# Kernel optimization log

Measured on AMD Instinct MI355X. Metric: run time of the kernel, lower is better.

## Reference

```python
import jax, jax.numpy as jnp
import numpy as np

D_MODEL = 512
N_HEADS = 8
NUM_NODES = 20
EPS = 1e-5

def _layer_norm(x, g, b):
    mu = jnp.mean(x, axis=-1, keepdims=True)
    var = jnp.var(x, axis=-1, keepdims=True)
    return (x - mu) * jax.lax.rsqrt(var + EPS) * g + b

def _conv1d(x_bcn, w_oik):
    # x: [B, C, N], w: [O, I, K], padding = K//2 (same)
    k = w_oik.shape[-1]
    p = k // 2
    return jax.lax.conv_general_dilated(
        x_bcn, w_oik, window_strides=(1,), padding=[(p, p)],
        dimension_numbers=('NCH', 'OIH', 'NCH'))

def setup_inputs() -> dict:
    key = jax.random.key(0)
    ks = jax.random.split(key, 6)
    B, N, D, H = 4096, NUM_NODES, D_MODEL, N_HEADS
    x = jax.random.normal(ks[0], (B, N, D), dtype=jnp.float32)
    s = 1.0 / np.sqrt(D * 3)
    Wq = jax.random.normal(ks[1], (D, D, 3), dtype=jnp.float32) * s
    Wk = jax.random.normal(ks[2], (D, D, 3), dtype=jnp.float32) * s
    Wv = jax.random.normal(ks[3], (D, D, 3), dtype=jnp.float32) * s
    rel_table = jax.random.normal(ks[4], (2 * N - 1, H), dtype=jnp.float32) * 0.02
    Wo = jax.random.normal(ks[5], (D, D), dtype=jnp.float32) * (1.0 / np.sqrt(D))
    bo = jnp.zeros((D,), dtype=jnp.float32)
    ones = jnp.ones((D,), dtype=jnp.float32)
    zeros = jnp.zeros((D,), dtype=jnp.float32)
    return {"x": x, "Wq": Wq, "Wk": Wk, "Wv": Wv,
            "lnq_g": ones, "lnq_b": zeros, "lnk_g": ones, "lnk_b": zeros,
            "lnv_g": ones, "lnv_b": zeros,
            "rel_table": rel_table, "Wo": Wo, "bo": bo}

def reference(x, Wq, Wk, Wv, lnq_g, lnq_b, lnk_g, lnk_b, lnv_g, lnv_b, rel_table, Wo, bo):
    B, N, D = x.shape
    H = N_HEADS
    dk = D // H
    x_p = jnp.transpose(x, (0, 2, 1))  # [B, D, N]

    def proj(W, g, b):
        c = _conv1d(x_p, W)                      # [B, D, N]
        c = _layer_norm(jnp.transpose(c, (0, 2, 1)), g, b)  # [B, N, D]
        return x + c                              # residual

    q = proj(Wq, lnq_g, lnq_b)
    k = proj(Wk, lnk_g, lnk_b)
    v = proj(Wv, lnv_g, lnv_b)

    q = q.reshape(B, N, H, dk).transpose(0, 2, 1, 3)  # [B,H,N,dk]
    k = k.reshape(B, N, H, dk).transpose(0, 2, 1, 3)
    v = v.reshape(B, N, H, dk).transpose(0, 2, 1, 3)

    scale = 1.0 / np.sqrt(dk)
    scores = jnp.einsum('bhnd,bhmd->bhnm', q, k) * scale  # [B,H,N,N]

    # relative position bias: index[i,j] = i - j + N - 1
    coords = jnp.arange(N)
    rel_idx = coords[:, None] - coords[None, :] + (N - 1)   # [N,N]
    rel_bias = rel_table[rel_idx]                            # [N,N,H]
    rel_bias = jnp.transpose(rel_bias, (2, 0, 1))[None]      # [1,H,N,N]
    scores = scores + rel_bias

    attn = jax.nn.softmax(scores, axis=-1)
    out = jnp.einsum('bhnm,bhmd->bhnd', attn, v)             # [B,H,N,dk]
    out = out.transpose(0, 2, 1, 3).reshape(B, N, D)
    return out @ Wo.T + bo
```

## Files before the change

kernel.cpp:

```cpp
#include <hip/hip_runtime.h>
#include <hip/hip_bf16.h>
#include <stdint.h>
#include <string.h>

typedef __attribute__((ext_vector_type(8))) __bf16 bf16x8;
typedef __attribute__((ext_vector_type(2))) __bf16 bf16x2;
typedef __attribute__((ext_vector_type(4))) float f32x4;
typedef __attribute__((ext_vector_type(16))) float f32x16;

#define B_TOT   4096
#define NN      20
#define DM      512
#define NC1     1536
#define M_TOT   (B_TOT*NN)
#define NPAD    22

__device__ __forceinline__ void async_copy16(const __bf16* g, __bf16* l) {
    __builtin_amdgcn_global_load_lds(
        (__attribute__((address_space(1))) void*)g,
        (__attribute__((address_space(3))) void*)l, 16, 0, 0);
}

template<typename T>
__device__ __forceinline__ void load8(const T* p, float* r) {
    if constexpr (sizeof(T) == 4) {
        f32x4 a = *(const f32x4*)p;
        f32x4 b = *(const f32x4*)(p + 4);
#pragma unroll
        for (int i = 0; i < 4; ++i) { r[i] = a[i]; r[i + 4] = b[i]; }
    } else {
        bf16x8 a = *(const bf16x8*)p;
#pragma unroll
        for (int i = 0; i < 8; ++i) r[i] = (float)a[i];
    }
}

__device__ __forceinline__ bf16x8 zero8() {
    bf16x8 z;
#pragma unroll
    for (int i = 0; i < 8; ++i) z[i] = (__bf16)0.f;
    return z;
}

__device__ __forceinline__ uint32_t pkbf(float a, float b) {
    __bf16 x = (__bf16)a, y = (__bf16)b;
    uint16_t ux, uy;
    __builtin_memcpy(&ux, &x, 2); __builtin_memcpy(&uy, &y, 2);
    return (uint32_t)ux | ((uint32_t)uy << 16);
}

__device__ __forceinline__ bf16x8 mkfrag(uint32_t w0, uint32_t w1, uint32_t w2, uint32_t w3) {
    union { uint32_t u[4]; bf16x8 v; } X;
    X.u[0] = w0; X.u[1] = w1; X.u[2] = w2; X.u[3] = w3;
    return X.v;
}

__global__ void detect_kernel(const uint32_t* __restrict__ xw, int* __restrict__ mode) {
    int lane = threadIdx.x & 63;
    int susp = 0;
#pragma unroll
    for (int i = 0; i < 4; ++i) {
        uint32_t w = xw[lane * 4 + i];
        uint32_t e = (w >> 7) & 0xFF;
        if ((e >= 118 && e <= 130) || (w & 0xFFFFu) == 0) susp++;
    }
#pragma unroll
    for (int o = 32; o > 0; o >>= 1) susp += __shfl_xor(susp, o, 64);
    if (lane == 0) *mode = (susp > 128) ? 1 : 0;
}

template<typename T>
__device__ __forceinline__ void wt_body(
    const T* __restrict__ Wq, const T* __restrict__ Wk, const T* __restrict__ Wv,
    const T* __restrict__ Wo, __bf16* __restrict__ Wt, __bf16* __restrict__ Wob, int t)
{
    if (t < 3 * 512 * 512) {
        int p = t >> 18;
        int r = t & 262143;
        int o = r >> 9, i = r & 511;
        const T* W = (p == 0) ? Wq : ((p == 1) ? Wk : Wv);
        const T* src = W + (size_t)(o * 512 + i) * 3;
        float w0 = (float)src[0], w1 = (float)src[1], w2 = (float)src[2];
        size_t base = (size_t)(p * 512 + o) * 1536 + i;
        Wt[base]        = (__bf16)w0;
        Wt[base + 512]  = (__bf16)w1;
        Wt[base + 1024] = (__bf16)w2;
    } else {
        int g2 = t - 3 * 512 * 512;
        Wob[g2] = (__bf16)(float)Wo[g2];
    }
}

__global__ __launch_bounds__(256) void wt_kernel(
    const void* Wq, const void* Wk, const void* Wv, const void* Wo,
    __bf16* Wt, __bf16* Wob, const int* mode)
{
    int t = blockIdx.x * 256 + threadIdx.x;
    if (*mode)
        wt_body<__bf16>((const __bf16*)Wq, (const __bf16*)Wk, (const __bf16*)Wv,
                        (const __bf16*)Wo, Wt, Wob, t);
    else
        wt_body<float>((const float*)Wq, (const float*)Wk, (const float*)Wv,
                       (const float*)Wo, Wt, Wob, t);
}

template<typename T>
__device__ __forceinline__ void xpad_body(
    const T* __restrict__ x, __bf16* __restrict__ xp, int idx)
{
    int col = (idx & 63) * 8;
    int row = idx >> 6;
    int b = row / 22;
    int np = row - b * 22;
    bf16x8 ov;
    if (np == 0 || np == 21) {
        ov = zero8();
    } else {
        float tmp[8];
        load8<T>(x + ((size_t)(b * 20 + np - 1) * 512 + col), tmp);
#pragma unroll
        for (int t = 0; t < 8; ++t) ov[t] = (__bf16)tmp[t];
    }
    *(bf16x8*)(xp + (size_t)row * 512 + col) = ov;
}

__global__ __launch_bounds__(256) void xpad_kernel(
    const void* x, __bf16* xp, const int* mode)
{
    int idx = blockIdx.x * 256 + threadIdx.x;
    if (*mode) xpad_body<__bf16>((const __bf16*)x, xp, idx);
    else       xpad_body<float>((const float*)x, xp, idx);
}

#define SBAR()  __builtin_amdgcn_s_barrier()
#define SCHED0() __builtin_amdgcn_sched_barrier(0)
#define LGKM0() do { asm volatile("s_waitcnt lgkmcnt(0)" ::: "memory"); SCHED0(); } while (0)
#define VM4()   do { SCHED0(); asm volatile("s_waitcnt vmcnt(4)" ::: "memory"); } while (0)
#define VM0()   do { SCHED0(); asm volatile("s_waitcnt vmcnt(0)" ::: "memory"); } while (0)

__device__ __forceinline__ void g1_loadA(const __bf16* slab, int off, bf16x8 (&aq)[4]) {
#pragma unroll
    for (int i = 0; i < 4; ++i) aq[i] = *(const bf16x8*)(slab + off + i * 512);
}
__device__ __forceinline__ void g1_loadB(const __bf16* slab, int off, bf16x8 (&bq)[4]) {
#pragma unroll
    for (int i = 0; i < 4; ++i) bq[i] = *(const bf16x8*)(slab + off + i * 512);
}
template<int QM>
__device__ __forceinline__ void g1_mma(bf16x8 (&aq)[4], bf16x8 (&bq)[4], f32x4 (&acc)[8][4]) {
    __builtin_amdgcn_s_setprio(1);
#pragma unroll
    for (int i = 0; i < 4; ++i)
#pragma unroll
        for (int nf = 0; nf < 4; ++nf)
            acc[QM * 4 + i][nf] = __builtin_amdgcn_mfma_f32_16x16x32_bf16(
                aq[i], bq[nf], acc[QM * 4 + i][nf], 0, 0, 0);
    __builtin_amdgcn_s_setprio(0);
}

template<int NT>
__device__ __forceinline__ void kloop8(
    const __bf16* aP0, const __bf16* aP1, const __bf16* bP0, const __bf16* bP1,
    __bf16* shA, __bf16* shB, int sdst, int rdA, int rdB, f32x4 (&acc)[8][4])
{
    bf16x8 aq[4], bq[4];
    { __bf16* d = shA + 0 * 8192 + sdst; async_copy16(aP0 + 0, d);  async_copy16(aP1 + 0, d + 4096); }
    { __bf16* d = shB + 0 * 8192 + sdst; async_copy16(bP0 + 0, d);  async_copy16(bP1 + 0, d + 4096); }
    { __bf16* d = shA + 1 * 8192 + sdst; async_copy16(aP0 + 32, d); async_copy16(aP1 + 32, d + 4096); }
    { __bf16* d = shB + 1 * 8192 + sdst; async_copy16(bP0 + 32, d); async_copy16(bP1 + 32, d + 4096); }
    VM4();
    SBAR();

    for (int t = 0; t < NT; ++t) {
        const int cur = t & 1;
        const __bf16* A0 = shA + (cur * 2 + 0) * 8192;
        const __bf16* A1 = shA + (cur * 2 + 1) * 8192;
        const __bf16* B0 = shB + (cur * 2 + 0) * 8192;
        const __bf16* B1 = shB + (cur * 2 + 1) * 8192;
        __bf16* dA0 = shA + ((cur ^ 1) * 2 + 0) * 8192 + sdst;
        __bf16* dA1 = shA + ((cur ^ 1) * 2 + 1) * 8192 + sdst;
        __bf16* dB0 = shB + ((cur ^ 1) * 2 + 0) * 8192 + sdst;
        __bf16* dB1 = shB + ((cur ^ 1) * 2 + 1) * 8192 + sdst;
        const int kn = (t + 1) * 64;
        const bool st = (t < NT - 1);

        g1_loadA(A0, rdA, aq);
        g1_loadB(B0, rdB, bq);
        if (st) { async_copy16(aP0 + kn, dA0); async_copy16(aP1 + kn, dA0 + 4096); }
        SBAR(); LGKM0();
        g1_mma<0>(aq, bq, acc);
        SBAR();

        g1_loadA(A0, rdA + 2048, aq);
        if (st) { async_copy16(bP0 + kn, dB0); async_copy16(bP1 + kn, dB0 + 4096); }
        if (st) VM4(); else VM0();
        SBAR(); LGKM0();
        g1_mma<1>(aq, bq, acc);
        SBAR();

        g1_loadA(A1, rdA, aq);
        g1_loadB(B1, rdB, bq);
        if (st) { async_copy16(aP0 + kn + 32, dA1); async_copy16(aP1 + kn + 32, dA1 + 4096); }
        SBAR(); LGKM0();
        g1_mma<0>(aq, bq, acc);
        SBAR();

        g1_loadA(A1, rdA + 2048, aq);
        if (st) { async_copy16(bP0 + kn + 32, dB1); async_copy16(bP1 + kn + 32, dB1 + 4096); }
        if (st) VM4();
        SBAR(); LGKM0();
        g1_mma<1>(aq, bq, acc);
        SBAR();
    }
}

__global__ __launch_bounds__(512, 2) void g1_kernel(
    const __bf16* __restrict__ xpad, const __bf16* __restrict__ Wt,
    __bf16* __restrict__ Cout, int mbase)
{
    extern __shared__ __align__(16) __bf16 sh[];
    __bf16* shA = sh;
    __bf16* shB = sh + 32768;

    const int tid = threadIdx.x;
    const int w = tid >> 6, l = tid & 63;
    const int lr = l & 15, lq = l >> 4;
    const int wm = w >> 2, wn = w & 3;

    int nwg = gridDim.x;
    int bid = blockIdx.x;
    if ((nwg & 7) == 0) bid = (bid & 7) * (nwg >> 3) + (bid >> 3);
    const int nb = bid % 6;
    const int mb = bid / 6;
    const int n0 = nb * 256;
    const int mloc = mb * 256;

    const int rin = l >> 2;
    const int pc  = (l & 3) * 8;
    const int lc  = (rin >= 8) ? (pc ^ 16) : pc;
    const int R0 = w * 16 + rin;
    const int R1 = 128 + R0;
    const int g0 = mbase + mloc + R0, g1r = mbase + mloc + R1;
    const __bf16* aP0 = xpad + (size_t)((g0 / 20) * 22 + g0 % 20) * 512 + lc;
    const __bf16* aP1 = xpad + (size_t)((g1r / 20) * 22 + g1r % 20) * 512 + lc;
    const __bf16* bP0 = Wt + (size_t)(n0 + R0) * 1536 + lc;
    const __bf16* bP1 = Wt + (size_t)(n0 + R1) * 1536 + lc;
    const int sdst = w * 512 + l * 8;

    const int swzcol = (lr >= 8) ? ((lq * 8) ^ 16) : (lq * 8);
    const int ardoff = lr * 32 + swzcol;
    const int rdA = wm * 8 * 512 + ardoff;
    const int rdB = wn * 4 * 512 + ardoff;

    f32x4 acc[8][4] = {};
    kloop8<24>(aP0, aP1, bP0, bP1, shA, shB, sdst, rdA, rdB, acc);

#pragma unroll
    for (int mf = 0; mf < 8; ++mf) {
#pragma unroll
        for (int r = 0; r < 4; ++r) {
            int row = mloc + wm * 128 + mf * 16 + lq * 4 + r;
            size_t base = (size_t)row * 1536 + n0 + wn * 64 + lr;
#pragma unroll
            for (int nf = 0; nf < 4; ++nf)
                Cout[base + nf * 16] = (__bf16)acc[mf][nf][r];
        }
    }
}

template<typename T>
__device__ __forceinline__ void attn_body(
    const __bf16* __restrict__ xpad, const __bf16* __restrict__ cqkv,
    const T* __restrict__ lnq_g, const T* __restrict__ lnq_b,
    const T* __restrict__ lnk_g, const T* __restrict__ lnk_b,
    const T* __restrict__ lnv_g, const T* __restrict__ lnv_b,
    const T* __restrict__ rel, __bf16* __restrict__ aout, int bbase,
    __bf16* sq , float* rbt , float* gbln )
{
    const int tid = threadIdx.x;
    const int wave = tid >> 6, lane = tid & 63;
    const int bl = blockIdx.x;
    char* sqb = (char*)sq;
    const size_t xpbase = ((size_t)(bbase + bl) * NPAD + 1) * DM;
    const size_t cbase = (size_t)bl * NN * NC1;

    if (tid < 384) {
        int idx = tid * 8;
        float tmp[8];
        if (idx < 1536) {
            int p = idx >> 9, col = idx & 511;
            const T* g = (p == 0) ? lnq_g : (p == 1) ? lnk_g : lnv_g;
            load8<T>(g + col, tmp);
        } else {
            int q2 = idx - 1536;
            int p = q2 >> 9, col = q2 & 511;
            const T* bb = (p == 0) ? lnq_b : (p == 1) ? lnk_b : lnv_b;
            load8<T>(bb + col, tmp);
        }
#pragma unroll
        for (int u = 0; u < 8; ++u) gbln[idx + u] = tmp[u];
    }
    if (tid < 312) {
        int h = tid & 7, d = tid >> 3;
        rbt[h * 40 + d] = (float)rel[tid];
    }
    __syncthreads();

    {
        int n0r = wave % 20;
        bf16x8 cv0 = *(const bf16x8*)(cqkv + cbase + (size_t)n0r * NC1 + 0 * 512 + lane * 8);
        bf16x8 xv0 = *(const bf16x8*)(xpad + xpbase + (size_t)n0r * DM + lane * 8);
#pragma unroll
        for (int rr = 0; rr < 8; ++rr) {
            int row = wave + rr * 8;
            if (row < 60) {
                int nrow = row + 8;
                bf16x8 cv1, xv1;
                if (nrow < 60) {
                    int p1 = nrow / 20, n1 = nrow - p1 * 20;
                    cv1 = *(const bf16x8*)(cqkv + cbase + (size_t)n1 * NC1 + p1 * 512 + lane * 8);
                    xv1 = *(const bf16x8*)(xpad + xpbase + (size_t)n1 * DM + lane * 8);
                }
                int p = row / 20;
                float vals[8]; float s1 = 0.f, s2 = 0.f;
#pragma unroll
                for (int t = 0; t < 8; ++t) { float f = (float)cv0[t]; vals[t] = f; s1 += f; s2 += f * f; }
#pragma unroll
                for (int o = 32; o > 0; o >>= 1) { s1 += __shfl_xor(s1, o, 64); s2 += __shfl_xor(s2, o, 64); }
                float mu = s1 * (1.f / 512.f);
                float var = s2 * (1.f / 512.f) - mu * mu;
                float rs = rsqrtf(var + 1e-5f);
                const float* gv = gbln + p * 512 + lane * 8;
                const float* bv = gbln + 1536 + p * 512 + lane * 8;
                bf16x8 ov;
#pragma unroll
                for (int t = 0; t < 8; ++t)
                    ov[t] = (__bf16)((vals[t] - mu) * rs * gv[t] + bv[t] + (float)xv0[t]);
                *(bf16x8*)(sqb + row * 1024 + ((lane * 16) ^ ((row & 7) << 4))) = ov;
                cv0 = cv1; xv0 = xv1;
            }
        }
    }
    __syncthreads();

    const int h  = wave;
    const int ic = lane & 31;
    const int lq = lane >> 5;

    f32x16 s;
#pragma unroll
    for (int r = 0; r < 16; ++r) s[r] = 0.f;
#pragma unroll
    for (int call = 0; call < 4; ++call) {
        int kb2 = (call * 16 + lq * 8) * 2;
        bf16x8 af = zero8(), bf_ = zero8();
        if (ic < 20) {
            int rk = 20 + ic;
            af  = *(const bf16x8*)(sqb + rk * 1024 + ((h * 128 + kb2) ^ ((rk & 7) << 4)));
            bf_ = *(const bf16x8*)(sqb + ic * 1024 + ((h * 128 + kb2) ^ ((ic & 7) << 4)));
        }
        s = __builtin_amdgcn_mfma_f32_32x32x16_bf16(af, bf_, s, 0, 0, 0);
    }
    __syncthreads();

    {
        float mx = -1e30f;
#pragma unroll
        for (int r = 0; r < 16; ++r) {
            int j = (r & 3) + 8 * (r >> 2) + 4 * lq;
            if (j < 20) {
                int d = ic - j + 19;
                d = d < 0 ? 0 : (d > 38 ? 38 : d);
                s[r] = s[r] * 0.125f + rbt[h * 40 + d];
                mx = fmaxf(mx, s[r]);
            } else s[r] = -1e30f;
        }
        mx = fmaxf(mx, __shfl_xor(mx, 32, 64));
        float sum = 0.f;
#pragma unroll
        for (int r = 0; r < 16; ++r) {
            int j = (r & 3) + 8 * (r >> 2) + 4 * lq;
            float e = (j < 20) ? __expf(s[r] - mx) : 0.f;
            s[r] = e; sum += e;
        }
        sum += __shfl_xor(sum, 32, 64);
        float inv = 1.f / sum;
#pragma unroll
        for (int r = 0; r < 16; ++r) s[r] *= inv;
    }

    bf16x8 pa1, pa2;
    {
        uint32_t pk[8], qk[8];
#pragma unroll
        for (int k = 0; k < 8; ++k) pk[k] = pkbf(s[2 * k], s[2 * k + 1]);
#pragma unroll
        for (int k = 0; k < 8; ++k) qk[k] = (uint32_t)__shfl_xor((int)pk[k], 32, 64);
        pa1 = lq ? mkfrag(qk[2], qk[3], pk[2], pk[3]) : mkfrag(pk[0], pk[1], qk[0], qk[1]);
        pa2 = lq ? mkfrag(qk[6], qk[7], pk[6], pk[7]) : mkfrag(pk[4], pk[5], qk[4], qk[5]);
    }

#pragma unroll 1
    for (int half = 0; half < 2; ++half) {
        f32x16 o;
#pragma unroll
        for (int r = 0; r < 16; ++r) o[r] = 0.f;
        const int cb2 = h * 128 + half * 64 + ic * 2;
#pragma unroll
        for (int call = 0; call < 2; ++call) {
            int jb = call * 16 + lq * 8;
            union { unsigned short u[8]; bf16x8 v; } V;
#pragma unroll
            for (int e = 0; e < 8; ++e) {
                int j = jb + e;
                unsigned short val = 0;
                if (j < 20) {
                    int rv = 40 + j;
                    val = *(const unsigned short*)(sqb + rv * 1024 + (cb2 ^ ((rv & 7) << 4)));
                }
                V.u[e] = val;
            }
            o = __builtin_amdgcn_mfma_f32_32x32x16_bf16(call ? pa2 : pa1, V.v, o, 0, 0, 0);
        }
#pragma unroll
        for (int r = 0; r < 16; ++r) {
            int i = (r & 3) + 8 * (r >> 2) + 4 * lq;
            if (i < 20) {
                __bf16 b = (__bf16)o[r];
                unsigned short ub;
                __builtin_memcpy(&ub, &b, 2);
                *(unsigned short*)(sqb + i * 1024 + (cb2 ^ ((i & 7) << 4))) = ub;
            }
        }
    }
    __syncthreads();

    __bf16* ab = aout + (size_t)bl * NN * DM;
    for (int t = tid; t < 1280; t += 512) {
        int row = t >> 6;
        int bc = (t & 63) * 16;
        bf16x8 vv = *(const bf16x8*)(sqb + row * 1024 + (bc ^ ((row & 7) << 4)));
        *(bf16x8*)(ab + t * 8) = vv;
    }
}

__global__ __launch_bounds__(512, 4) void attn_kernel(
    const __bf16* xpad, const __bf16* cqkv,
    const void* lnq_g, const void* lnq_b, const void* lnk_g, const void* lnk_b,
    const void* lnv_g, const void* lnv_b, const void* rel,
    __bf16* aout, int bbase, const int* mode)
{
    __shared__ __align__(16) __bf16 sq[60 * 512];
    __shared__ float rbt[8 * 40];
    __shared__ float gbln[3072];
    if (*mode)
        attn_body<__bf16>(xpad, cqkv,
            (const __bf16*)lnq_g, (const __bf16*)lnq_b, (const __bf16*)lnk_g,
            (const __bf16*)lnk_b, (const __bf16*)lnv_g, (const __bf16*)lnv_b,
            (const __bf16*)rel, aout, bbase, sq, rbt, gbln);
    else
        attn_body<float>(xpad, cqkv,
            (const float*)lnq_g, (const float*)lnq_b, (const float*)lnk_g,
            (const float*)lnk_b, (const float*)lnv_g, (const float*)lnv_b,
            (const float*)rel, aout, bbase, sq, rbt, gbln);
}

template<typename T>
__device__ __forceinline__ void g3_body(
    const __bf16* __restrict__ Ain, const __bf16* __restrict__ Wob,
    const T* __restrict__ bo, T* __restrict__ out, int mbase, __bf16* sh)
{
    __bf16* shA = sh;
    __bf16* shB = sh + 32768;

    const int tid = threadIdx.x;
    const int w = tid >> 6, l = tid & 63;
    const int lr = l & 15, lq = l >> 4;
    const int wm = w >> 2, wn = w & 3;

    int nwg = gridDim.x;
    int bid = blockIdx.x;
    if ((nwg & 7) == 0) bid = (bid & 7) * (nwg >> 3) + (bid >> 3);
    const int nb = bid & 1;
    const int mb = bid >> 1;
    const int n0 = nb * 256;
    const int mloc = mb * 256;

    const int rin = l >> 2;
    const int pc  = (l & 3) * 8;
    const int lc  = (rin >= 8) ? (pc ^ 16) : pc;
    const int R0 = w * 16 + rin;
    const int R1 = 128 + R0;
    const __bf16* aP0 = Ain + (size_t)(mloc + R0) * 512 + lc;
    const __bf16* aP1 = Ain + (size_t)(mloc + R1) * 512 + lc;
    const __bf16* bP0 = Wob + (size_t)(n0 + R0) * 512 + lc;
    const __bf16* bP1 = Wob + (size_t)(n0 + R1) * 512 + lc;
    const int sdst = w * 512 + l * 8;

    const int swzcol = (lr >= 8) ? ((lq * 8) ^ 16) : (lq * 8);
    const int ardoff = lr * 32 + swzcol;
    const int rdA = wm * 8 * 512 + ardoff;
    const int rdB = wn * 4 * 512 + ardoff;

    f32x4 acc[8][4] = {};
    kloop8<8>(aP0, aP1, bP0, bP1, shA, shB, sdst, rdA, rdB, acc);

    float bias[4];
#pragma unroll
    for (int nf = 0; nf < 4; ++nf) bias[nf] = (float)bo[n0 + wn * 64 + lr + nf * 16];
#pragma unroll
    for (int mf = 0; mf < 8; ++mf) {
#pragma unroll
        for (int r = 0; r < 4; ++r) {
            int row = mloc + wm * 128 + mf * 16 + lq * 4 + r;
            size_t gbase = (size_t)(mbase + row) * 512 + n0 + wn * 64 + lr;
#pragma unroll
            for (int nf = 0; nf < 4; ++nf)
                out[gbase + nf * 16] = (T)(acc[mf][nf][r] + bias[nf]);
        }
    }
}

__global__ __launch_bounds__(512, 2) void g3_kernel(
    const __bf16* Ain, const __bf16* Wob, const void* bo, void* out,
    int mbase, const int* mode)
{
    extern __shared__ __align__(16) __bf16 sh3[];
    if (*mode) g3_body<__bf16>(Ain, Wob, (const __bf16*)bo, (__bf16*)out, mbase, sh3);
    else       g3_body<float>(Ain, Wob, (const float*)bo, (float*)out, mbase, sh3);
}

extern "C" void kernel_launch(void* const* d_in, const int* in_sizes, int n_in,
                              void* d_out, int out_size, void* d_ws, size_t ws_size,
                              hipStream_t stream) {
    (void)in_sizes; (void)n_in; (void)out_size;
    char* ws = (char*)d_ws;
    int*    mode = (int*)ws;
    __bf16* Wt   = (__bf16*)(ws + 256);
    __bf16* Wob  = (__bf16*)(ws + 256 + 4718592);
    __bf16* xpad = (__bf16*)(ws + 256 + 4718592 + 524288);
    const size_t off_c = 256 + 4718592 + 524288 + (size_t)B_TOT * NPAD * DM * 2;

    static bool attr_set = false;
    if (!attr_set) {
        (void)hipFuncSetAttribute((const void*)g1_kernel,
                                  hipFuncAttributeMaxDynamicSharedMemorySize, 131072);
        (void)hipFuncSetAttribute((const void*)g3_kernel,
                                  hipFuncAttributeMaxDynamicSharedMemorySize, 131072);
        attr_set = true;
    }

    int CH = 2;
    while (CH < 64) {
        size_t rows = (size_t)M_TOT / CH;
        if (off_c + rows * (size_t)NC1 * 2 + rows * (size_t)DM * 2 <= ws_size) break;
        CH *= 2;
    }
    const int rows = M_TOT / CH;
    const int Bc   = B_TOT / CH;
    __bf16* Cbuf = (__bf16*)(ws + off_c);
    __bf16* Abuf = (__bf16*)(ws + off_c + (size_t)rows * NC1 * 2);

    detect_kernel<<<dim3(1), dim3(64), 0, stream>>>((const uint32_t*)d_in[0], mode);
    wt_kernel<<<dim3(4096), dim3(256), 0, stream>>>(
        d_in[1], d_in[2], d_in[3], d_in[11], Wt, Wob, mode);
    xpad_kernel<<<dim3(22528), dim3(256), 0, stream>>>(d_in[0], xpad, mode);

    for (int c = 0; c < CH; ++c) {
        int mbase = c * rows;
        g1_kernel<<<dim3(6 * (rows / 256)), dim3(512), 131072, stream>>>(
            xpad, Wt, Cbuf, mbase);
        attn_kernel<<<dim3(Bc), dim3(512), 0, stream>>>(
            xpad, Cbuf, d_in[4], d_in[5], d_in[6], d_in[7], d_in[8], d_in[9],
            d_in[10], Abuf, mbase / NN, mode);
        g3_kernel<<<dim3(2 * (rows / 256)), dim3(512), 131072, stream>>>(
            Abuf, Wob, d_in[12], d_out, mbase, mode);
    }
}
```

Before: 843.0 us.

## Store V transposed in LDS, drop LN param staging, launch unchunked

V rows are written to a separate transposed, swizzled LDS buffer, so the P·V MFMA reads V fragments as two vector loads instead of sixteen scalar gathers and writes outputs as 4-wide stores. LayerNorm gamma/beta are now loaded per row straight from global memory instead of being staged in shared memory. The chunked launch loop is replaced by single full-size launches of the three kernels, which removes launch overhead but drops the workspace-size check and assumes the workspace can hold the whole intermediate buffers.

```diff
diff --git a/kernel.cpp b/kernel.cpp
--- a/kernel.cpp
+++ b/kernel.cpp
@@ -4,7 +4,7 @@
 #include <string.h>
 
 typedef __attribute__((ext_vector_type(8))) __bf16 bf16x8;
-typedef __attribute__((ext_vector_type(2))) __bf16 bf16x2;
+typedef __attribute__((ext_vector_type(4))) __bf16 bf16x4;
 typedef __attribute__((ext_vector_type(4))) float f32x4;
 typedef __attribute__((ext_vector_type(16))) float f32x16;
 
@@ -275,31 +275,20 @@
     const T* __restrict__ lnk_g, const T* __restrict__ lnk_b,
     const T* __restrict__ lnv_g, const T* __restrict__ lnv_b,
     const T* __restrict__ rel, __bf16* __restrict__ aout, int bbase,
-    __bf16* sq , float* rbt , float* gbln )
+    __bf16* sq , __bf16* vT ,
+    float* rbt )
 {
     const int tid = threadIdx.x;
     const int wave = tid >> 6, lane = tid & 63;
     const int bl = blockIdx.x;
     char* sqb = (char*)sq;
+    char* vTb = (char*)vT;
     const size_t xpbase = ((size_t)(bbase + bl) * NPAD + 1) * DM;
     const size_t cbase = (size_t)bl * NN * NC1;
 
-    if (tid < 384) {
-        int idx = tid * 8;
-        float tmp[8];
-        if (idx < 1536) {
-            int p = idx >> 9, col = idx & 511;
-            const T* g = (p == 0) ? lnq_g : (p == 1) ? lnk_g : lnv_g;
-            load8<T>(g + col, tmp);
-        } else {
-            int q2 = idx - 1536;
-            int p = q2 >> 9, col = q2 & 511;
-            const T* bb = (p == 0) ? lnq_b : (p == 1) ? lnk_b : lnv_b;
-            load8<T>(bb + col, tmp);
-        }
-#pragma unroll
-        for (int u = 0; u < 8; ++u) gbln[idx + u] = tmp[u];
-    }
+#pragma unroll
+    for (int k = 0; k < 4; ++k)
+        *(bf16x8*)(vTb + tid * 64 + k * 16) = zero8();
     if (tid < 312) {
         int h = tid & 7, d = tid >> 3;
         rbt[h * 40 + d] = (float)rel[tid];
@@ -322,6 +311,7 @@
                     xv1 = *(const bf16x8*)(xpad + xpbase + (size_t)n1 * DM + lane * 8);
                 }
                 int p = row / 20;
+                int n = row - p * 20;
                 float vals[8]; float s1 = 0.f, s2 = 0.f;
 #pragma unroll
                 for (int t = 0; t < 8; ++t) { float f = (float)cv0[t]; vals[t] = f; s1 += f; s2 += f * f; }
@@ -330,13 +320,27 @@
                 float mu = s1 * (1.f / 512.f);
                 float var = s2 * (1.f / 512.f) - mu * mu;
                 float rs = rsqrtf(var + 1e-5f);
-                const float* gv = gbln + p * 512 + lane * 8;
-                const float* bv = gbln + 1536 + p * 512 + lane * 8;
+                const T* g  = (p == 0) ? lnq_g : (p == 1) ? lnk_g : lnv_g;
+                const T* bb = (p == 0) ? lnq_b : (p == 1) ? lnk_b : lnv_b;
+                float gv[8], bv[8];
+                load8<T>(g  + lane * 8, gv);
+                load8<T>(bb + lane * 8, bv);
                 bf16x8 ov;
 #pragma unroll
                 for (int t = 0; t < 8; ++t)
                     ov[t] = (__bf16)((vals[t] - mu) * rs * gv[t] + bv[t] + (float)xv0[t]);
-                *(bf16x8*)(sqb + row * 1024 + ((lane * 16) ^ ((row & 7) << 4))) = ov;
+                if (p < 2) {
+                    *(bf16x8*)(sqb + row * 1024 + ((lane * 16) ^ ((row & 7) << 4))) = ov;
+                } else {
+#pragma unroll
+                    for (int t = 0; t < 8; ++t) {
+                        int c = lane * 8 + t;
+                        unsigned short ub;
+                        __bf16 b = ov[t];
+                        __builtin_memcpy(&ub, &b, 2);
+                        *(unsigned short*)(vTb + c * 64 + ((n * 2) ^ (((c >> 3) & 3) << 4))) = ub;
+                    }
+                }
                 cv0 = cv1; xv0 = xv1;
             }
         }
@@ -401,35 +405,26 @@
     }
 
 #pragma unroll 1
-    for (int half = 0; half < 2; ++half) {
+    for (int ct = 0; ct < 2; ++ct) {
+        const int cbase = h * 64 + ct * 32;
+        const int c_a = cbase + ic;
+        const int arow = c_a * 64;
+        const int aswz = ((c_a >> 3) & 3) << 4;
+        bf16x8 a1 = *(const bf16x8*)(vTb + arow + ((lq * 16 + 0)  ^ aswz));
+        bf16x8 a2 = *(const bf16x8*)(vTb + arow + ((lq * 16 + 32) ^ aswz));
         f32x16 o;
 #pragma unroll
         for (int r = 0; r < 16; ++r) o[r] = 0.f;
-        const int cb2 = h * 128 + half * 64 + ic * 2;
-#pragma unroll
-        for (int call = 0; call < 2; ++call) {
-            int jb = call * 16 + lq * 8;
-            union { unsigned short u[8]; bf16x8 v; } V;
-#pragma unroll
-            for (int e = 0; e < 8; ++e) {
-                int j = jb + e;
-                unsigned short val = 0;
-                if (j < 20) {
-                    int rv = 40 + j;
-                    val = *(const unsigned short*)(sqb + rv * 1024 + (cb2 ^ ((rv & 7) << 4)));
-                }
-                V.u[e] = val;
-            }
-            o = __builtin_amdgcn_mfma_f32_32x32x16_bf16(call ? pa2 : pa1, V.v, o, 0, 0, 0);
-        }
-#pragma unroll
-        for (int r = 0; r < 16; ++r) {
-            int i = (r & 3) + 8 * (r >> 2) + 4 * lq;
-            if (i < 20) {
-                __bf16 b = (__bf16)o[r];
-                unsigned short ub;
-                __builtin_memcpy(&ub, &b, 2);
-                *(unsigned short*)(sqb + i * 1024 + (cb2 ^ ((i & 7) << 4))) = ub;
+        o = __builtin_amdgcn_mfma_f32_32x32x16_bf16(a1, pa1, o, 0, 0, 0);
+        o = __builtin_amdgcn_mfma_f32_32x32x16_bf16(a2, pa2, o, 0, 0, 0);
+        if (ic < 20) {
+#pragma unroll
+            for (int g2 = 0; g2 < 4; ++g2) {
+                int c0 = cbase + 8 * g2 + 4 * lq;
+                bf16x4 ov4;
+#pragma unroll
+                for (int e = 0; e < 4; ++e) ov4[e] = (__bf16)o[g2 * 4 + e];
+                *(bf16x4*)(sqb + ic * 1024 + ((c0 * 2) ^ ((ic & 7) << 4))) = ov4;
             }
         }
     }
@@ -450,19 +445,19 @@
     const void* lnv_g, const void* lnv_b, const void* rel,
     __bf16* aout, int bbase, const int* mode)
 {
-    __shared__ __align__(16) __bf16 sq[60 * 512];
+    __shared__ __align__(16) __bf16 sq[40 * 512];
+    __shared__ __align__(16) __bf16 vT[512 * 32];
     __shared__ float rbt[8 * 40];
-    __shared__ float gbln[3072];
     if (*mode)
         attn_body<__bf16>(xpad, cqkv,
             (const __bf16*)lnq_g, (const __bf16*)lnq_b, (const __bf16*)lnk_g,
             (const __bf16*)lnk_b, (const __bf16*)lnv_g, (const __bf16*)lnv_b,
-            (const __bf16*)rel, aout, bbase, sq, rbt, gbln);
+            (const __bf16*)rel, aout, bbase, sq, vT, rbt);
     else
         attn_body<float>(xpad, cqkv,
             (const float*)lnq_g, (const float*)lnq_b, (const float*)lnk_g,
             (const float*)lnk_b, (const float*)lnv_g, (const float*)lnv_b,
-            (const float*)rel, aout, bbase, sq, rbt, gbln);
+            (const float*)rel, aout, bbase, sq, vT, rbt);
 }
 
 template<typename T>
@@ -533,7 +528,7 @@
 extern "C" void kernel_launch(void* const* d_in, const int* in_sizes, int n_in,
                               void* d_out, int out_size, void* d_ws, size_t ws_size,
                               hipStream_t stream) {
-    (void)in_sizes; (void)n_in; (void)out_size;
+    (void)in_sizes; (void)n_in; (void)out_size; (void)ws_size;
     char* ws = (char*)d_ws;
     int*    mode = (int*)ws;
     __bf16* Wt   = (__bf16*)(ws + 256);
@@ -550,30 +545,19 @@
         attr_set = true;
     }
 
-    int CH = 2;
-    while (CH < 64) {
-        size_t rows = (size_t)M_TOT / CH;
-        if (off_c + rows * (size_t)NC1 * 2 + rows * (size_t)DM * 2 <= ws_size) break;
-        CH *= 2;
-    }
-    const int rows = M_TOT / CH;
-    const int Bc   = B_TOT / CH;
     __bf16* Cbuf = (__bf16*)(ws + off_c);
-    __bf16* Abuf = (__bf16*)(ws + off_c + (size_t)rows * NC1 * 2);
+    __bf16* Abuf = (__bf16*)(ws + off_c + (size_t)M_TOT * NC1 * 2);
 
     detect_kernel<<<dim3(1), dim3(64), 0, stream>>>((const uint32_t*)d_in[0], mode);
     wt_kernel<<<dim3(4096), dim3(256), 0, stream>>>(
         d_in[1], d_in[2], d_in[3], d_in[11], Wt, Wob, mode);
     xpad_kernel<<<dim3(22528), dim3(256), 0, stream>>>(d_in[0], xpad, mode);
 
-    for (int c = 0; c < CH; ++c) {
-        int mbase = c * rows;
-        g1_kernel<<<dim3(6 * (rows / 256)), dim3(512), 131072, stream>>>(
-            xpad, Wt, Cbuf, mbase);
-        attn_kernel<<<dim3(Bc), dim3(512), 0, stream>>>(
-            xpad, Cbuf, d_in[4], d_in[5], d_in[6], d_in[7], d_in[8], d_in[9],
-            d_in[10], Abuf, mbase / NN, mode);
-        g3_kernel<<<dim3(2 * (rows / 256)), dim3(512), 131072, stream>>>(
-            Abuf, Wob, d_in[12], d_out, mbase, mode);
-    }
-}
+    g1_kernel<<<dim3(6 * (M_TOT / 256)), dim3(512), 131072, stream>>>(
+        xpad, Wt, Cbuf, 0);
+    attn_kernel<<<dim3(B_TOT), dim3(512), 0, stream>>>(
+        xpad, Cbuf, d_in[4], d_in[5], d_in[6], d_in[7], d_in[8], d_in[9],
+        d_in[10], Abuf, 0, mode);
+    g3_kernel<<<dim3(2 * (M_TOT / 256)), dim3(512), 131072, stream>>>(
+        Abuf, Wob, d_in[12], d_out, 0, mode);
+}
```

Measured after the change: 815.8 us. 3.2% less time.
